# Optimization experiments

Measured on AMD Instinct MI355X. Metric: run time of the kernel, lower is better.

## Reference

```python
import jax, jax.numpy as jnp
import numpy as np

ALPHA = 0.2  # LeakyReLU negative slope
NEG_INF = -9e15


def setup_inputs() -> dict:
    key = jax.random.key(0)
    k_h, k_adj, k_W, k_a = jax.random.split(key, 4)
    B, N, Din, Dout = 8, 1024, 256, 256
    h = jax.random.normal(k_h, (B, N, Din), dtype=jnp.float32)
    adj = jax.random.randint(k_adj, (B, N, N), 0, 2, dtype=jnp.int32)
    # nn.Linear weight [out, in], xavier-uniform-ish init for a
    W = jax.random.normal(k_W, (Dout, Din), dtype=jnp.float32) * (1.0 / np.sqrt(Din))
    lim = np.float32(1.414 * np.sqrt(6.0 / (2 * Dout + 1)))
    a = jax.random.uniform(k_a, (2 * Dout, 1), dtype=jnp.float32, minval=-lim, maxval=lim)
    return {"h": h, "adj": adj, "W": W, "a": a}


def reference(h, adj, W, a):
    # Wh: [B, N, F]
    Wh = jnp.einsum('bnd,fd->bnf', h, W)
    F_ = Wh.shape[-1]
    # Decompose concat-then-matmul: e_ij = leakyrelu(Wh_i @ a1 + Wh_j @ a2)
    a1 = a[:F_, 0]   # [F]
    a2 = a[F_:, 0]   # [F]
    src = Wh @ a1    # [B, N]  score contribution of row node i
    dst = Wh @ a2    # [B, N]  score contribution of col node j
    e = src[:, :, None] + dst[:, None, :]          # [B, N, N]
    e = jnp.where(e > 0, e, ALPHA * e)             # LeakyReLU
    e = jnp.where(adj > 0, e, NEG_INF)             # mask non-edges
    attention = jax.nn.softmax(e, axis=-1)         # [B, N, N]
    # dropout p=0.0 -> identity in eval/train
    h_prime = jnp.einsum('bij,bjf->bif', attention, Wh)
    return h_prime
```

## Files before the change

### kernel.cpp

```cpp
#include <hip/hip_runtime.h>
#include <hip/hip_bf16.h>
#include <cstdint>

#define ALPHA 0.2f
#define NEG_INF -9000000000000000.0f

typedef __bf16 bf16_t;
typedef __bf16 bf16x4 __attribute__((ext_vector_type(4)));
typedef __bf16 bf16x8 __attribute__((ext_vector_type(8)));
typedef float f32x16 __attribute__((ext_vector_type(16)));

__global__ __launch_bounds__(256) void k_gemm1(
    const float* __restrict__ h, const float* __restrict__ W, bf16_t* __restrict__ WhT)
{
  __shared__ bf16_t WS[64 * 72];
  __shared__ bf16_t HS[64 * 72];
  const int bx = blockIdx.x;
  const int b  = bx & 7;
  const int jt = (bx >> 3) & 15;
  const int ft = bx >> 7;
  const int j0 = jt * 64, f0 = ft * 64;
  const int t = threadIdx.x;
  const int w = t >> 6, lane = t & 63;
  const int mrow = lane & 31, half = lane >> 5;
  const int fsub = (w & 1) * 32, jsub = (w >> 1) * 32;

  const int lr = t >> 2;
  const int lc = (t & 3) * 16;
  const float* wp = W + ((size_t)(f0 + lr)) * 256 + lc;
  const float* hp = h + ((size_t)(b * 1024 + j0 + lr)) * 256 + lc;

  f32x16 acc;
#pragma unroll
  for (int r = 0; r < 16; r++) acc[r] = 0.f;

  for (int s = 0; s < 4; s++) {
    if (s) __syncthreads();
    {
      float4 w0 = *(const float4*)(wp + s * 64);
      float4 w1 = *(const float4*)(wp + s * 64 + 4);
      float4 w2 = *(const float4*)(wp + s * 64 + 8);
      float4 w3 = *(const float4*)(wp + s * 64 + 12);
      bf16x8 va, vb;
      va[0] = (bf16_t)w0.x; va[1] = (bf16_t)w0.y; va[2] = (bf16_t)w0.z; va[3] = (bf16_t)w0.w;
      va[4] = (bf16_t)w1.x; va[5] = (bf16_t)w1.y; va[6] = (bf16_t)w1.z; va[7] = (bf16_t)w1.w;
      vb[0] = (bf16_t)w2.x; vb[1] = (bf16_t)w2.y; vb[2] = (bf16_t)w2.z; vb[3] = (bf16_t)w2.w;
      vb[4] = (bf16_t)w3.x; vb[5] = (bf16_t)w3.y; vb[6] = (bf16_t)w3.z; vb[7] = (bf16_t)w3.w;
      *(bf16x8*)&WS[lr * 72 + lc] = va;
      *(bf16x8*)&WS[lr * 72 + lc + 8] = vb;
      float4 h0 = *(const float4*)(hp + s * 64);
      float4 h1 = *(const float4*)(hp + s * 64 + 4);
      float4 h2 = *(const float4*)(hp + s * 64 + 8);
      float4 h3 = *(const float4*)(hp + s * 64 + 12);
      bf16x8 vc, vd;
      vc[0] = (bf16_t)h0.x; vc[1] = (bf16_t)h0.y; vc[2] = (bf16_t)h0.z; vc[3] = (bf16_t)h0.w;
      vc[4] = (bf16_t)h1.x; vc[5] = (bf16_t)h1.y; vc[6] = (bf16_t)h1.z; vc[7] = (bf16_t)h1.w;
      vd[0] = (bf16_t)h2.x; vd[1] = (bf16_t)h2.y; vd[2] = (bf16_t)h2.z; vd[3] = (bf16_t)h2.w;
      vd[4] = (bf16_t)h3.x; vd[5] = (bf16_t)h3.y; vd[6] = (bf16_t)h3.z; vd[7] = (bf16_t)h3.w;
      *(bf16x8*)&HS[lr * 72 + lc] = vc;
      *(bf16x8*)&HS[lr * 72 + lc + 8] = vd;
    }
    __syncthreads();
#pragma unroll
    for (int ks = 0; ks < 4; ks++) {
      bf16x8 af = *(const bf16x8*)&WS[(fsub + mrow) * 72 + ks * 16 + half * 8];
      bf16x8 bf = *(const bf16x8*)&HS[(jsub + mrow) * 72 + ks * 16 + half * 8];
      acc = __builtin_amdgcn_mfma_f32_32x32x16_bf16(af, bf, acc, 0, 0, 0);
    }
  }

  const int jcol = j0 + jsub + mrow;
#pragma unroll
  for (int r = 0; r < 16; r++) {
    int frow = fsub + (r & 3) + 8 * (r >> 2) + 4 * half;
    WhT[(((size_t)(b * 256 + f0 + frow)) << 10) + jcol] = (bf16_t)acc[r];
  }
}

__global__ __launch_bounds__(256) void k_src(
    const float* __restrict__ h, const float* __restrict__ W, const float* __restrict__ a,
    float* __restrict__ src, float* __restrict__ dst)
{
  __shared__ float uS[512];
  const int t = threadIdx.x;
  {
    float s1a = 0.f, s1b = 0.f, s2a = 0.f, s2b = 0.f;
#pragma unroll 4
    for (int f = 0; f < 256; f += 2) {
      float w0 = W[f * 256 + t];
      float w1 = W[(f + 1) * 256 + t];
      s1a = fmaf(w0, a[f], s1a);       s1b = fmaf(w1, a[f + 1], s1b);
      s2a = fmaf(w0, a[256 + f], s2a); s2b = fmaf(w1, a[256 + f + 1], s2b);
    }
    uS[t] = s1a + s1b; uS[256 + t] = s2a + s2b;
  }
  __syncthreads();
  const int n = t >> 4, c = t & 15;
  const int m = blockIdx.x * 16 + n;
  const float* hp = h + (size_t)m * 256 + c * 16;
  float s1 = 0.f, s2 = 0.f;
#pragma unroll
  for (int i = 0; i < 4; i++) {
    float4 v = *(const float4*)(hp + i * 4);
    const float* u1p = &uS[c * 16 + i * 4];
    const float* u2p = &uS[256 + c * 16 + i * 4];
    s1 = fmaf(v.x, u1p[0], s1); s1 = fmaf(v.y, u1p[1], s1);
    s1 = fmaf(v.z, u1p[2], s1); s1 = fmaf(v.w, u1p[3], s1);
    s2 = fmaf(v.x, u2p[0], s2); s2 = fmaf(v.y, u2p[1], s2);
    s2 = fmaf(v.z, u2p[2], s2); s2 = fmaf(v.w, u2p[3], s2);
  }
#pragma unroll
  for (int off = 8; off; off >>= 1) {
    s1 += __shfl_down(s1, off, 16);
    s2 += __shfl_down(s2, off, 16);
  }
  if (c == 0) { src[m] = s1; dst[m] = s2; }
}

__global__ __launch_bounds__(256) void k_stats(
    const int* __restrict__ adj, const float* __restrict__ src, const float* __restrict__ dst,
    bf16_t* __restrict__ P, float* __restrict__ linv_ws)
{
  const int b  = blockIdx.x & 7;
  const int i0 = (blockIdx.x >> 3) << 2;
  const int t  = threadIdx.x;
  const int wv = t >> 6, lane = t & 63;
  __shared__ float dstS[1024];
  __shared__ float srcS[4];
  __shared__ float partL[4][4];
  *(float4*)&dstS[t * 4] = *(const float4*)(dst + (b << 10) + t * 4);
  if (t < 4) srcS[t] = src[(b << 10) + i0 + t];
  __syncthreads();

  const float4 dj = *(const float4*)&dstS[4 * t];
  for (int i = 0; i < 4; i++) {
    const float si = srcS[i];
    const size_t row = (size_t)(b << 10) + i0 + i;
    const int4 av = *(const int4*)(adj + (row << 10) + 4 * t);
    float v0 = si + dj.x, v1 = si + dj.y, v2 = si + dj.z, v3 = si + dj.w;
    float e0 = (av.x > 0) ? fmaxf(v0, ALPHA * v0) : NEG_INF;
    float e1 = (av.y > 0) ? fmaxf(v1, ALPHA * v1) : NEG_INF;
    float e2 = (av.z > 0) ? fmaxf(v2, ALPHA * v2) : NEG_INF;
    float e3 = (av.w > 0) ? fmaxf(v3, ALPHA * v3) : NEG_INF;
    float x0 = __expf(e0), x1 = __expf(e1), x2 = __expf(e2), x3 = __expf(e3);
    bf16x4 pv;
    pv[0] = (bf16_t)x0; pv[1] = (bf16_t)x1; pv[2] = (bf16_t)x2; pv[3] = (bf16_t)x3;
    *(bf16x4*)(P + (row << 10) + 4 * t) = pv;
    float lt = (x0 + x1) + (x2 + x3);
#pragma unroll
    for (int off = 32; off; off >>= 1)
      lt += __shfl_down(lt, off, 64);
    if (lane == 0) partL[i][wv] = lt;
  }
  __syncthreads();
  if (t < 4) {
    float L = (partL[t][0] + partL[t][1]) + (partL[t][2] + partL[t][3]);
    linv_ws[(b << 10) + i0 + t] = 1.0f / L;
  }
}

__global__ __launch_bounds__(256) void k_attn(
    const bf16_t* __restrict__ P, const bf16_t* __restrict__ WhT,
    const float* __restrict__ linv_ws, float* __restrict__ out)
{
  const int b  = blockIdx.x & 7;
  const int fh = (blockIdx.x >> 3) & 1;
  const int i0 = (blockIdx.x >> 4) << 5;
  const int t  = threadIdx.x;
  const int w  = t >> 6;
  const int lane = t & 63;
  const int mrow = lane & 31, half = lane >> 5;

  const bf16_t* ap = P + (((size_t)((b << 10) + i0 + mrow)) << 10) + half * 8;
  const bf16_t* bp = WhT + (((size_t)(b * 256 + fh * 128 + w * 32 + mrow)) << 10) + half * 8;

  f32x16 acc;
#pragma unroll
  for (int r = 0; r < 16; r++) acc[r] = 0.f;

#pragma unroll 8
  for (int idx = 0; idx < 64; idx++) {
    bf16x8 afr = *(const bf16x8*)(ap + idx * 16);
    bf16x8 bfr = *(const bf16x8*)(bp + idx * 16);
    acc = __builtin_amdgcn_mfma_f32_32x32x16_bf16(afr, bfr, acc, 0, 0, 0);
  }

  const int col = fh * 128 + w * 32 + mrow;
  const float* lp = linv_ws + (b << 10) + i0;
#pragma unroll
  for (int r = 0; r < 16; r++) {
    int row = (r & 3) + 8 * (r >> 2) + 4 * half;
    out[((size_t)(b << 10) + i0 + row) * 256 + col] = acc[r] * lp[row];
  }
}

extern "C" void kernel_launch(void* const* d_in, const int* in_sizes, int n_in,
                              void* d_out, int out_size, void* d_ws, size_t ws_size,
                              hipStream_t stream) {
  const float* h   = (const float*)d_in[0];
  const int*   adj = (const int*)d_in[1];
  const float* W   = (const float*)d_in[2];
  const float* a   = (const float*)d_in[3];
  float* out = (float*)d_out;

  char* wsb = (char*)d_ws;
  bf16_t* WhT = (bf16_t*)wsb;
  bf16_t* P   = (bf16_t*)(wsb + (4u << 20));
  float* srcv = (float*)(wsb + (20u << 20));
  float* dstv = srcv + 8192;
  float* linv = srcv + 16384;

  k_src  <<<512,  256, 0, stream>>>(h, W, a, srcv, dstv);
  k_gemm1<<<512,  256, 0, stream>>>(h, W, WhT);
  k_stats<<<2048, 256, 0, stream>>>(adj, srcv, dstv, P, linv);
  k_attn <<<512,  256, 0, stream>>>(P, WhT, linv, out);
}
```

Measured before the change: 137.5 us.

## Fuse attention-score computation and softmax-weighted GEMM into one kernel

```diff
diff --git a/kernel.cpp b/kernel.cpp
--- a/kernel.cpp
+++ b/kernel.cpp
@@ -6,7 +6,6 @@
 #define NEG_INF -9000000000000000.0f
 
 typedef __bf16 bf16_t;
-typedef __bf16 bf16x4 __attribute__((ext_vector_type(4)));
 typedef __bf16 bf16x8 __attribute__((ext_vector_type(8)));
 typedef float f32x16 __attribute__((ext_vector_type(16)));
 
@@ -117,51 +116,10 @@
   if (c == 0) { src[m] = s1; dst[m] = s2; }
 }
 
-__global__ __launch_bounds__(256) void k_stats(
-    const int* __restrict__ adj, const float* __restrict__ src, const float* __restrict__ dst,
-    bf16_t* __restrict__ P, float* __restrict__ linv_ws)
-{
-  const int b  = blockIdx.x & 7;
-  const int i0 = (blockIdx.x >> 3) << 2;
-  const int t  = threadIdx.x;
-  const int wv = t >> 6, lane = t & 63;
-  __shared__ float dstS[1024];
-  __shared__ float srcS[4];
-  __shared__ float partL[4][4];
-  *(float4*)&dstS[t * 4] = *(const float4*)(dst + (b << 10) + t * 4);
-  if (t < 4) srcS[t] = src[(b << 10) + i0 + t];
-  __syncthreads();
-
-  const float4 dj = *(const float4*)&dstS[4 * t];
-  for (int i = 0; i < 4; i++) {
-    const float si = srcS[i];
-    const size_t row = (size_t)(b << 10) + i0 + i;
-    const int4 av = *(const int4*)(adj + (row << 10) + 4 * t);
-    float v0 = si + dj.x, v1 = si + dj.y, v2 = si + dj.z, v3 = si + dj.w;
-    float e0 = (av.x > 0) ? fmaxf(v0, ALPHA * v0) : NEG_INF;
-    float e1 = (av.y > 0) ? fmaxf(v1, ALPHA * v1) : NEG_INF;
-    float e2 = (av.z > 0) ? fmaxf(v2, ALPHA * v2) : NEG_INF;
-    float e3 = (av.w > 0) ? fmaxf(v3, ALPHA * v3) : NEG_INF;
-    float x0 = __expf(e0), x1 = __expf(e1), x2 = __expf(e2), x3 = __expf(e3);
-    bf16x4 pv;
-    pv[0] = (bf16_t)x0; pv[1] = (bf16_t)x1; pv[2] = (bf16_t)x2; pv[3] = (bf16_t)x3;
-    *(bf16x4*)(P + (row << 10) + 4 * t) = pv;
-    float lt = (x0 + x1) + (x2 + x3);
-#pragma unroll
-    for (int off = 32; off; off >>= 1)
-      lt += __shfl_down(lt, off, 64);
-    if (lane == 0) partL[i][wv] = lt;
-  }
-  __syncthreads();
-  if (t < 4) {
-    float L = (partL[t][0] + partL[t][1]) + (partL[t][2] + partL[t][3]);
-    linv_ws[(b << 10) + i0 + t] = 1.0f / L;
-  }
-}
-
-__global__ __launch_bounds__(256) void k_attn(
-    const bf16_t* __restrict__ P, const bf16_t* __restrict__ WhT,
-    const float* __restrict__ linv_ws, float* __restrict__ out)
+__global__ __launch_bounds__(256) void k_fused(
+    const bf16_t* __restrict__ WhT, const int* __restrict__ adj,
+    const float* __restrict__ src, const float* __restrict__ dst,
+    float* __restrict__ out)
 {
   const int b  = blockIdx.x & 7;
   const int fh = (blockIdx.x >> 3) & 1;
@@ -171,26 +129,57 @@
   const int lane = t & 63;
   const int mrow = lane & 31, half = lane >> 5;
 
-  const bf16_t* ap = P + (((size_t)((b << 10) + i0 + mrow)) << 10) + half * 8;
-  const bf16_t* bp = WhT + (((size_t)(b * 256 + fh * 128 + w * 32 + mrow)) << 10) + half * 8;
-
-  f32x16 acc;
-#pragma unroll
-  for (int r = 0; r < 16; r++) acc[r] = 0.f;
-
+  __shared__ float dstS[1024];
+  __shared__ float srcS[32];
+  __shared__ bf16_t P[2][32 * 264];
+
+  *(float4*)&dstS[t * 4] = *(const float4*)(dst + (b << 10) + t * 4);
+  if (t < 32) srcS[t] = src[(b << 10) + i0 + t];
+  __syncthreads();
+
+  f32x16 acc, acc2;
+#pragma unroll
+  for (int r = 0; r < 16; r++) { acc[r] = 0.f; acc2[r] = 0.f; }
+
+  bf16x8 ones;
+#pragma unroll
+  for (int k = 0; k < 8; k++) ones[k] = (bf16_t)1.0f;
+
+  const bf16_t* bp = WhT + (((size_t)(b * 256 + fh * 128 + w * 32 + mrow)) << 10);
+  const int* arow = adj + ((((size_t)(b << 10)) + i0) << 10) + t;
+
+  for (int c = 0; c < 4; c++) {
+    bf16_t* Pc = &P[c & 1][0];
+    {
+      float dj = dstS[c * 256 + t];
+      const int* ac = arow + c * 256;
 #pragma unroll 8
-  for (int idx = 0; idx < 64; idx++) {
-    bf16x8 afr = *(const bf16x8*)(ap + idx * 16);
-    bf16x8 bfr = *(const bf16x8*)(bp + idx * 16);
-    acc = __builtin_amdgcn_mfma_f32_32x32x16_bf16(afr, bfr, acc, 0, 0, 0);
+      for (int i = 0; i < 32; i++) {
+        int av = ac[(size_t)i << 10];
+        float v = srcS[i] + dj;
+        float vl = fmaxf(v, ALPHA * v);
+        float e = (av > 0) ? vl : NEG_INF;
+        Pc[i * 264 + t] = (bf16_t)__expf(e);
+      }
+    }
+    __syncthreads();
+
+    const bf16_t* bpc = bp + c * 256 + half * 8;
+    const bf16_t* prow = Pc + mrow * 264 + half * 8;
+#pragma unroll
+    for (int idx = 0; idx < 16; idx++) {
+      bf16x8 afr = *(const bf16x8*)(prow + idx * 16);
+      bf16x8 bfr = *(const bf16x8*)(bpc + idx * 16);
+      acc  = __builtin_amdgcn_mfma_f32_32x32x16_bf16(afr, bfr, acc, 0, 0, 0);
+      acc2 = __builtin_amdgcn_mfma_f32_32x32x16_bf16(afr, ones, acc2, 0, 0, 0);
+    }
   }
 
   const int col = fh * 128 + w * 32 + mrow;
-  const float* lp = linv_ws + (b << 10) + i0;
 #pragma unroll
   for (int r = 0; r < 16; r++) {
     int row = (r & 3) + 8 * (r >> 2) + 4 * half;
-    out[((size_t)(b << 10) + i0 + row) * 256 + col] = acc[r] * lp[row];
+    out[((size_t)(b << 10) + i0 + row) * 256 + col] = acc[r] / acc2[r];
   }
 }
 
@@ -205,13 +194,10 @@
 
   char* wsb = (char*)d_ws;
   bf16_t* WhT = (bf16_t*)wsb;
-  bf16_t* P   = (bf16_t*)(wsb + (4u << 20));
-  float* srcv = (float*)(wsb + (20u << 20));
+  float* srcv = (float*)(wsb + (4u << 20));
   float* dstv = srcv + 8192;
-  float* linv = srcv + 16384;
-
-  k_src  <<<512,  256, 0, stream>>>(h, W, a, srcv, dstv);
-  k_gemm1<<<512,  256, 0, stream>>>(h, W, WhT);
-  k_stats<<<2048, 256, 0, stream>>>(adj, srcv, dstv, P, linv);
-  k_attn <<<512,  256, 0, stream>>>(P, WhT, linv, out);
-}
+
+  k_src  <<<512, 256, 0, stream>>>(h, W, a, srcv, dstv);
+  k_gemm1<<<512, 256, 0, stream>>>(h, W, WhT);
+  k_fused<<<512, 256, 0, stream>>>(WhT, adj, srcv, dstv, out);
+}
```

Result: no change. 139.0 us (+1.1%).
